# Optimization experiments

Measured on AMD Instinct MI355X. Metric: run time of the kernel, lower is better.

Reference implementation:

```python
import jax, jax.numpy as jnp
import numpy as np

B, S, D, H = 2, 2048, 1024, 16
HD = D // H  # head dim = 64

def setup_inputs() -> dict:
    key = jax.random.key(0)
    k1, k2, k3 = jax.random.split(key, 3)
    return {
        "hidden_state": jax.random.normal(k1, (B, S, D), dtype=jnp.float32),
        "attention_mask": jnp.ones((B, S), dtype=jnp.float32),
        "w_attn": jax.random.normal(k2, (D, 3 * D), dtype=jnp.float32) * 0.02,
        "b_attn": jnp.zeros((3 * D,), dtype=jnp.float32),
        "w_proj": jax.random.normal(k3, (D, D), dtype=jnp.float32) * 0.02,
        "b_proj": jnp.zeros((D,), dtype=jnp.float32),
    }

def reference(hidden_state, attention_mask, w_attn, b_attn, w_proj, b_proj):
    x = hidden_state  # [B,S,D]
    # Conv1D: F.linear(x, weight.T, bias) == x @ weight + bias
    qkv = x @ w_attn + b_attn  # [B,S,3D]
    q, k, v = jnp.split(qkv, 3, axis=-1)
    def heads(t):  # [B,S,D] -> [B,H,S,HD]
        return t.reshape(B, S, H, HD).transpose(0, 2, 1, 3)
    q, k, v = heads(q), heads(k), heads(v)
    # scaled scores
    scores = jnp.einsum("bhqd,bhkd->bhqk", q, k) / jnp.sqrt(jnp.float32(HD))
    # mask: expand (B,S)->(B,S,S) along keys, tril, 1-that, !=0 -> -inf
    m = jnp.broadcast_to(attention_mask[:, None, :], (B, S, S))
    neg = 1.0 - jnp.tril(m)  # nonzero where disallowed
    bias = jnp.where(neg != 0.0, -jnp.inf, 0.0)  # [B,S,S]
    scores = scores + bias[:, None, :, :]
    attn = jax.nn.softmax(scores, axis=-1)  # [B,H,S,S] (dropout p=0)
    ctx = jnp.einsum("bhqk,bhkd->bhqd", attn, v)  # [B,H,S,HD]
    ctx = ctx.transpose(0, 2, 1, 3).reshape(B, S, D)
    out = ctx @ w_proj + b_proj  # resid dropout p=0
    # original returns attention.transpose(0,1): (H,B,S,S)->(B,H,S,S)
    return out, attn
```

## Files before the change

kernel.cpp:

```cpp
#include <hip/hip_runtime.h>

#define S_ 2048
#define D_ 1024
#define H_ 16
#define HD_ 64

typedef __attribute__((ext_vector_type(8))) short short8;
typedef __attribute__((ext_vector_type(4))) float floatx4;

#define MFMA16(a, b, c) __builtin_amdgcn_mfma_f32_16x16x32_bf16(a, b, c, 0, 0, 0)

__device__ inline unsigned short f2bf(float f) {
    union { float f; unsigned int u; } v; v.f = f;
    unsigned int r = v.u + 0x7FFFu + ((v.u >> 16) & 1u);
    return (unsigned short)(r >> 16);
}

__global__ __launch_bounds__(256) void cast_bf16(const float* __restrict__ in,
                                                 unsigned short* __restrict__ out, int n4) {
    int i = blockIdx.x * 256 + threadIdx.x;
    if (i < n4) {
        float4 v = ((const float4*)in)[i];
        ushort4 o;
        o.x = f2bf(v.x); o.y = f2bf(v.y); o.z = f2bf(v.z); o.w = f2bf(v.w);
        ((ushort4*)out)[i] = o;
    }
}

__global__ __launch_bounds__(256) void transpose_cast(const float* __restrict__ W,
                                                      unsigned short* __restrict__ WT,
                                                      int K, int N) {
    __shared__ float tb[64][65];
    const int t = threadIdx.x;
    const int tr = t >> 4, tc = t & 15;
    const int n0 = blockIdx.x * 64, k0 = blockIdx.y * 64;
#pragma unroll
    for (int p = 0; p < 4; ++p) {
        const int r = p * 16 + tr;
        const float4 v = *(const float4*)&W[(size_t)(k0 + r) * N + n0 + tc * 4];
        tb[r][tc * 4 + 0] = v.x; tb[r][tc * 4 + 1] = v.y;
        tb[r][tc * 4 + 2] = v.z; tb[r][tc * 4 + 3] = v.w;
    }
    __syncthreads();
#pragma unroll
    for (int p = 0; p < 4; ++p) {
        const int rn = p * 16 + tr;
        ushort4 o;
        o.x = f2bf(tb[tc * 4 + 0][rn]); o.y = f2bf(tb[tc * 4 + 1][rn]);
        o.z = f2bf(tb[tc * 4 + 2][rn]); o.w = f2bf(tb[tc * 4 + 3][rn]);
        *(ushort4*)&WT[(size_t)(n0 + rn) * K + k0 + tc * 4] = o;
    }
}

__global__ __launch_bounds__(256) void gemm_bt(
    const unsigned short* __restrict__ A, const unsigned short* __restrict__ Bt,
    const float* __restrict__ bias, float* __restrict__ outp,
    unsigned short* __restrict__ qw, unsigned short* __restrict__ kw,
    unsigned short* __restrict__ vtw, int M, int N, int K, int mode)
{
    __shared__ unsigned short As[128 * 32];
    __shared__ unsigned short Bs[128 * 32];

    const int tid = threadIdx.x;
    const int w = tid >> 6, lane = tid & 63;
    const int l15 = lane & 15, qd = lane >> 4;
    const int wr = w >> 1, wc = w & 1;
    const int row0 = blockIdx.y * 128, col0 = blockIdx.x * 128;

    floatx4 acc[4][4];
#pragma unroll
    for (int i = 0; i < 4; ++i)
#pragma unroll
        for (int j = 0; j < 4; ++j) acc[i][j] = (floatx4){0.f, 0.f, 0.f, 0.f};

    for (int k0 = 0; k0 < K; k0 += 32) {
        __syncthreads();
#pragma unroll
        for (int p = 0; p < 2; ++p) {
            const int c = p * 256 + tid;
            const int row = c >> 2, part = c & 3;
            *(uint4*)&As[row * 32 + part * 8] =
                *(const uint4*)&A[(size_t)(row0 + row) * K + k0 + part * 8];
            *(uint4*)&Bs[row * 32 + part * 8] =
                *(const uint4*)&Bt[(size_t)(col0 + row) * K + k0 + part * 8];
        }
        __syncthreads();
        short8 af[4], bfr[4];
#pragma unroll
        for (int mi = 0; mi < 4; ++mi)
            af[mi] = *(const short8*)&As[(wr * 64 + mi * 16 + l15) * 32 + qd * 8];
#pragma unroll
        for (int ni = 0; ni < 4; ++ni)
            bfr[ni] = *(const short8*)&Bs[(wc * 64 + ni * 16 + l15) * 32 + qd * 8];
#pragma unroll
        for (int mi = 0; mi < 4; ++mi)
#pragma unroll
            for (int ni = 0; ni < 4; ++ni)
                acc[mi][ni] = MFMA16(af[mi], bfr[ni], acc[mi][ni]);
    }

#pragma unroll
    for (int mi = 0; mi < 4; ++mi)
#pragma unroll
        for (int ni = 0; ni < 4; ++ni) {
            const int col = col0 + wc * 64 + ni * 16 + l15;
            const float bv = bias[col];
#pragma unroll
            for (int r = 0; r < 4; ++r) {
                const int row = row0 + wr * 64 + mi * 16 + qd * 4 + r;
                const float v = acc[mi][ni][r] + bv;
                if (mode == 0) {
                    outp[(size_t)row * N + col] = v;
                } else {
                    const int region = col >> 10;
                    const int hh = (col >> 6) & 15;
                    const int dd = col & 63;
                    const int bb = row >> 11;
                    const int ss = row & 2047;
                    const unsigned short bvv = f2bf(v);
                    if (region == 0)
                        qw[((size_t)(bb * 16 + hh) * 2048 + ss) * 64 + dd] = bvv;
                    else if (region == 1)
                        kw[((size_t)(bb * 16 + hh) * 2048 + ss) * 64 + dd] = bvv;
                    else
                        vtw[((size_t)(bb * 16 + hh) * 64 + dd) * 2048 + ss] = bvv;
                }
            }
        }
}

__global__ __launch_bounds__(256) void attn_mfma(
    const unsigned short* __restrict__ qg, const unsigned short* __restrict__ kg,
    const unsigned short* __restrict__ vtg, const float* __restrict__ mask,
    float* __restrict__ attnOut, unsigned short* __restrict__ ctxOut)
{
    __shared__ unsigned short Qs[64 * 72];
    __shared__ unsigned short Ks[64 * 72];
    __shared__ unsigned short Vt[64 * 72];
    __shared__ unsigned short Ps[64 * 80];
    __shared__ float maskS[64];

    const int tid = threadIdx.x;
    const int w = tid >> 6, lane = tid & 63;
    const int l15 = lane & 15, qd = lane >> 4;
    const int x = blockIdx.x;
    const int bh = x & 31;
    const int qt = 31 - (x >> 5);
    const int b = bh >> 4, h = bh & 15;
    const size_t base = (size_t)bh * (S_ * HD_);

#pragma unroll
    for (int p = 0; p < 2; ++p) {
        const int c = p * 256 + tid;
        const int row = c >> 3, part = c & 7;
        *(uint4*)&Qs[row * 72 + part * 8] =
            *(const uint4*)&qg[base + (size_t)(qt * 64 + row) * 64 + part * 8];
    }
    __syncthreads();
    const short8 aq0 = *(const short8*)&Qs[(w * 16 + l15) * 72 + 0 + qd * 8];
    const short8 aq1 = *(const short8*)&Qs[(w * 16 + l15) * 72 + 32 + qd * 8];

    const int qrow_base = qt * 64 + w * 16 + qd * 4;
    float m_i[4], l_i[4], rl[4];
#pragma unroll
    for (int r = 0; r < 4; ++r) { m_i[r] = -3e38f; l_i[r] = 0.f; }

    for (int jt = 0; jt <= qt; ++jt) {
        __syncthreads();
#pragma unroll
        for (int p = 0; p < 2; ++p) {
            const int c = p * 256 + tid;
            const int row = c >> 3, part = c & 7;
            *(uint4*)&Ks[row * 72 + part * 8] =
                *(const uint4*)&kg[base + (size_t)(jt * 64 + row) * 64 + part * 8];
        }
        if (tid < 64) maskS[tid] = mask[b * S_ + jt * 64 + tid];
        __syncthreads();

        float sv[4][4];
#pragma unroll
        for (int ni = 0; ni < 4; ++ni) {
            const short8 bk0 = *(const short8*)&Ks[(ni * 16 + l15) * 72 + 0 + qd * 8];
            const short8 bk1 = *(const short8*)&Ks[(ni * 16 + l15) * 72 + 32 + qd * 8];
            floatx4 s = {0.f, 0.f, 0.f, 0.f};
            s = MFMA16(aq0, bk0, s);
            s = MFMA16(aq1, bk1, s);
#pragma unroll
            for (int r = 0; r < 4; ++r) sv[ni][r] = s[r] * 0.125f;
        }
#pragma unroll
        for (int r = 0; r < 4; ++r) {
            const int qrow = qrow_base + r;
            float svr[4], tm = -3e38f;
#pragma unroll
            for (int ni = 0; ni < 4; ++ni) {
                const int col = jt * 64 + ni * 16 + l15;
                const bool ok = (col <= qrow) && (maskS[ni * 16 + l15] == 1.0f);
                svr[ni] = ok ? sv[ni][r] : -3e38f;
                tm = fmaxf(tm, svr[ni]);
            }
            if (tm > -1e37f) {
                const float mn = fmaxf(m_i[r], tm);
                const float sum = __expf(svr[0] - mn) + __expf(svr[1] - mn) +
                                  __expf(svr[2] - mn) + __expf(svr[3] - mn);
                l_i[r] = l_i[r] * __expf(m_i[r] - mn) + sum;
                m_i[r] = mn;
            }
        }
    }

#pragma unroll
    for (int r = 0; r < 4; ++r) {
        float m = m_i[r], l = l_i[r];
#pragma unroll
        for (int off = 1; off < 16; off <<= 1) {
            const float mo = __shfl_xor(m, off);
            const float lo = __shfl_xor(l, off);
            const float mn = fmaxf(m, mo);
            l = l * __expf(m - mn) + lo * __expf(mo - mn);
            m = mn;
        }
        m_i[r] = m;
        rl[r] = 1.0f / l;
    }

    floatx4 ctxa[4];
#pragma unroll
    for (int ni = 0; ni < 4; ++ni) ctxa[ni] = (floatx4){0.f, 0.f, 0.f, 0.f};
    float* attnBH = attnOut + (size_t)bh * S_ * S_;

    for (int jt = 0; jt < 32; ++jt) {
        if (jt <= qt) {
            __syncthreads();
#pragma unroll
            for (int p = 0; p < 2; ++p) {
                const int c = p * 256 + tid;
                const int row = c >> 3, part = c & 7;
                *(uint4*)&Ks[row * 72 + part * 8] =
                    *(const uint4*)&kg[base + (size_t)(jt * 64 + row) * 64 + part * 8];
                *(uint4*)&Vt[row * 72 + part * 8] =
                    *(const uint4*)&vtg[base + (size_t)row * S_ + jt * 64 + part * 8];
            }
            if (tid < 64) maskS[tid] = mask[b * S_ + jt * 64 + tid];
            __syncthreads();

            float sv[4][4];
#pragma unroll
            for (int ni = 0; ni < 4; ++ni) {
                const short8 bk0 = *(const short8*)&Ks[(ni * 16 + l15) * 72 + 0 + qd * 8];
                const short8 bk1 = *(const short8*)&Ks[(ni * 16 + l15) * 72 + 32 + qd * 8];
                floatx4 s = {0.f, 0.f, 0.f, 0.f};
                s = MFMA16(aq0, bk0, s);
                s = MFMA16(aq1, bk1, s);
#pragma unroll
                for (int r = 0; r < 4; ++r) sv[ni][r] = s[r] * 0.125f;
            }
#pragma unroll
            for (int ni = 0; ni < 4; ++ni) {
#pragma unroll
                for (int r = 0; r < 4; ++r) {
                    const int qrow = qrow_base + r;
                    const int col = jt * 64 + ni * 16 + l15;
                    const bool ok = (col <= qrow) && (maskS[ni * 16 + l15] == 1.0f);
                    const float p = ok ? __expf(sv[ni][r] - m_i[r]) * rl[r] : 0.0f;
                    attnBH[(size_t)qrow * S_ + col] = p;
                    Ps[(w * 16 + qd * 4 + r) * 80 + ni * 16 + l15] = f2bf(p);
                }
            }
            __syncthreads();
#pragma unroll
            for (int kk = 0; kk < 2; ++kk) {
                const short8 ap = *(const short8*)&Ps[(w * 16 + l15) * 80 + kk * 32 + qd * 8];
#pragma unroll
                for (int ni = 0; ni < 4; ++ni) {
                    const short8 bv = *(const short8*)&Vt[(ni * 16 + l15) * 72 + kk * 32 + qd * 8];
                    ctxa[ni] = MFMA16(ap, bv, ctxa[ni]);
                }
            }
        } else {
            const float4 z = {0.f, 0.f, 0.f, 0.f};
#pragma unroll
            for (int p = 0; p < 4; ++p) {
                const int c = p * 256 + tid;
                const int row = c >> 4, part = c & 15;
                *(float4*)&attnBH[(size_t)(qt * 64 + row) * S_ + jt * 64 + part * 4] = z;
            }
        }
    }

#pragma unroll
    for (int ni = 0; ni < 4; ++ni)
#pragma unroll
        for (int r = 0; r < 4; ++r) {
            const int qrow = qrow_base + r;
            ctxOut[((size_t)(b * S_ + qrow)) * D_ + h * 64 + ni * 16 + l15] =
                f2bf(ctxa[ni][r]);
        }
}

extern "C" void kernel_launch(void* const* d_in, const int* in_sizes, int n_in,
                              void* d_out, int out_size, void* d_ws, size_t ws_size,
                              hipStream_t stream) {
    const float* hidden = (const float*)d_in[0];
    const float* mask   = (const float*)d_in[1];
    const float* w_attn = (const float*)d_in[2];
    const float* b_attn = (const float*)d_in[3];
    const float* w_proj = (const float*)d_in[4];
    const float* b_proj = (const float*)d_in[5];

    float* out = (float*)d_out;
    float* attnOut = out + (size_t)2 * S_ * D_;

    unsigned short* ws = (unsigned short*)d_ws;
    const size_t E = (size_t)2 * S_ * D_;
    unsigned short* Xb   = ws;
    unsigned short* WaT  = Xb + E;
    unsigned short* WpT  = WaT + (size_t)3 * D_ * D_;
    unsigned short* qw   = WpT + (size_t)D_ * D_;
    unsigned short* kw   = qw + E;
    unsigned short* vtw  = kw + E;
    unsigned short* ctxb = vtw + E;

    dim3 blk(256);
    cast_bf16<<<dim3((int)(E / 4 / 256)), blk, 0, stream>>>(hidden, Xb, (int)(E / 4));
    transpose_cast<<<dim3(3 * D_ / 64, D_ / 64), blk, 0, stream>>>(w_attn, WaT, D_, 3 * D_);
    transpose_cast<<<dim3(D_ / 64, D_ / 64), blk, 0, stream>>>(w_proj, WpT, D_, D_);

    gemm_bt<<<dim3(3 * D_ / 128, 2 * S_ / 128), blk, 0, stream>>>(
        Xb, WaT, b_attn, nullptr, qw, kw, vtw, 2 * S_, 3 * D_, D_, 1);

    attn_mfma<<<dim3(2 * H_ * (S_ / 64)), blk, 0, stream>>>(
        qw, kw, vtw, mask, attnOut, ctxb);

    gemm_bt<<<dim3(D_ / 128, 2 * S_ / 128), blk, 0, stream>>>(
        ctxb, WpT, b_proj, out, nullptr, nullptr, nullptr, 2 * S_, D_, D_, 0);
}
```

Before: 748.6 us.

## Double-buffer GEMM and attention tiles via direct global-to-LDS loads with swizzle

Replaces register-staged shared-memory loads in the GEMM and attention kernels with global_load_lds direct copies into double-buffered, XOR-swizzled LDS tiles. The next K/V tile is prefetched while the current one is computed. Softmax switches to exp2 with a log2e-folded scale, and the causal compare is skipped off the diagonal tile. The large attention-probability and output writes become nontemporal stores, and MFMA sections get raised wave priority. These aim to hide global-load latency and cut LDS bank conflicts and write-cache pollution. The cost is extra LDS use and reliance on correct async-load synchronization.

After: 740.3 us. Within noise of the previous version (-1.1%).

```diff
diff --git a/kernel.cpp b/kernel.cpp
--- a/kernel.cpp
+++ b/kernel.cpp
@@ -9,11 +9,18 @@
 typedef __attribute__((ext_vector_type(4))) float floatx4;
 
 #define MFMA16(a, b, c) __builtin_amdgcn_mfma_f32_16x16x32_bf16(a, b, c, 0, 0, 0)
-
-__device__ inline unsigned short f2bf(float f) {
+#define EXP2 __builtin_amdgcn_exp2f
+
+__device__ __forceinline__ unsigned short f2bf(float f) {
     union { float f; unsigned int u; } v; v.f = f;
     unsigned int r = v.u + 0x7FFFu + ((v.u >> 16) & 1u);
     return (unsigned short)(r >> 16);
+}
+
+__device__ __forceinline__ void gll16(const unsigned short* g, unsigned short* l) {
+    __builtin_amdgcn_global_load_lds(
+        (const __attribute__((address_space(1))) void*)g,
+        (__attribute__((address_space(3))) void*)l, 16, 0, 0);
 }
 
 __global__ __launch_bounds__(256) void cast_bf16(const float* __restrict__ in,
@@ -58,8 +65,8 @@
     unsigned short* __restrict__ qw, unsigned short* __restrict__ kw,
     unsigned short* __restrict__ vtw, int M, int N, int K, int mode)
 {
-    __shared__ unsigned short As[128 * 32];
-    __shared__ unsigned short Bs[128 * 32];
+    __shared__ unsigned short As[2][128 * 32];
+    __shared__ unsigned short Bs[2][128 * 32];
 
     const int tid = threadIdx.x;
     const int w = tid >> 6, lane = tid & 63;
@@ -73,25 +80,38 @@
 #pragma unroll
         for (int j = 0; j < 4; ++j) acc[i][j] = (floatx4){0.f, 0.f, 0.f, 0.f};
 
-    for (int k0 = 0; k0 < K; k0 += 32) {
+    const int sr = tid >> 2;
+    const int gs = (tid & 3) ^ ((tid >> 3) & 3);
+    const unsigned short* Ab0 = A + (size_t)(row0 + sr) * K + gs * 8;
+    const unsigned short* Ab1 = A + (size_t)(row0 + 64 + sr) * K + gs * 8;
+    const unsigned short* Bb0 = Bt + (size_t)(col0 + sr) * K + gs * 8;
+    const unsigned short* Bb1 = Bt + (size_t)(col0 + 64 + sr) * K + gs * 8;
+
+    auto stage = [&](int bi, int k0) {
+        gll16(Ab0 + k0, &As[bi][tid * 8]);
+        gll16(Ab1 + k0, &As[bi][(256 + tid) * 8]);
+        gll16(Bb0 + k0, &Bs[bi][tid * 8]);
+        gll16(Bb1 + k0, &Bs[bi][(256 + tid) * 8]);
+    };
+
+    stage(0, 0);
+    const int nk = K >> 5;
+    for (int it = 0; it < nk; ++it) {
         __syncthreads();
-#pragma unroll
-        for (int p = 0; p < 2; ++p) {
-            const int c = p * 256 + tid;
-            const int row = c >> 2, part = c & 3;
-            *(uint4*)&As[row * 32 + part * 8] =
-                *(const uint4*)&A[(size_t)(row0 + row) * K + k0 + part * 8];
-            *(uint4*)&Bs[row * 32 + part * 8] =
-                *(const uint4*)&Bt[(size_t)(col0 + row) * K + k0 + part * 8];
-        }
-        __syncthreads();
+        if (it + 1 < nk) stage((it + 1) & 1, (it + 1) << 5);
+        const unsigned short* Asb = As[it & 1];
+        const unsigned short* Bsb = Bs[it & 1];
         short8 af[4], bfr[4];
 #pragma unroll
-        for (int mi = 0; mi < 4; ++mi)
-            af[mi] = *(const short8*)&As[(wr * 64 + mi * 16 + l15) * 32 + qd * 8];
-#pragma unroll
-        for (int ni = 0; ni < 4; ++ni)
-            bfr[ni] = *(const short8*)&Bs[(wc * 64 + ni * 16 + l15) * 32 + qd * 8];
+        for (int mi = 0; mi < 4; ++mi) {
+            const int ra = wr * 64 + mi * 16 + l15;
+            af[mi] = *(const short8*)&Asb[ra * 32 + ((qd ^ ((ra >> 1) & 3)) << 3)];
+        }
+#pragma unroll
+        for (int ni = 0; ni < 4; ++ni) {
+            const int rb = wc * 64 + ni * 16 + l15;
+            bfr[ni] = *(const short8*)&Bsb[rb * 32 + ((qd ^ ((rb >> 1) & 3)) << 3)];
+        }
 #pragma unroll
         for (int mi = 0; mi < 4; ++mi)
 #pragma unroll
@@ -110,7 +130,7 @@
                 const int row = row0 + wr * 64 + mi * 16 + qd * 4 + r;
                 const float v = acc[mi][ni][r] + bv;
                 if (mode == 0) {
-                    outp[(size_t)row * N + col] = v;
+                    __builtin_nontemporal_store(v, &outp[(size_t)row * N + col]);
                 } else {
                     const int region = col >> 10;
                     const int hh = (col >> 6) & 15;
@@ -134,11 +154,11 @@
     const unsigned short* __restrict__ vtg, const float* __restrict__ mask,
     float* __restrict__ attnOut, unsigned short* __restrict__ ctxOut)
 {
-    __shared__ unsigned short Qs[64 * 72];
-    __shared__ unsigned short Ks[64 * 72];
-    __shared__ unsigned short Vt[64 * 72];
+    __shared__ unsigned short Qb[64 * 64];
+    __shared__ unsigned short Kb[2][64 * 64];
+    __shared__ unsigned short Vb[2][64 * 64];
     __shared__ unsigned short Ps[64 * 80];
-    __shared__ float maskS[64];
+    __shared__ float maskS[2][64];
 
     const int tid = threadIdx.x;
     const int w = tid >> 6, lane = tid & 63;
@@ -148,17 +168,35 @@
     const int qt = 31 - (x >> 5);
     const int b = bh >> 4, h = bh & 15;
     const size_t base = (size_t)bh * (S_ * HD_);
-
-#pragma unroll
-    for (int p = 0; p < 2; ++p) {
-        const int c = p * 256 + tid;
-        const int row = c >> 3, part = c & 7;
-        *(uint4*)&Qs[row * 72 + part * 8] =
-            *(const uint4*)&qg[base + (size_t)(qt * 64 + row) * 64 + part * 8];
-    }
+    const float SC = 0.18033688f;
+
+    const int sr = tid >> 3;
+    const int sp = tid & 7;
+    const int gsw = sp ^ (sr & 7);
+
+    auto stageK = [&](int bi, int jt) {
+        const unsigned short* gk = kg + base + (size_t)jt * 4096;
+        gll16(gk + sr * 64 + gsw * 8, &Kb[bi][tid * 8]);
+        gll16(gk + (sr + 32) * 64 + gsw * 8, &Kb[bi][(256 + tid) * 8]);
+    };
+    auto stageV = [&](int bi, int jt) {
+        const unsigned short* gv = vtg + base + jt * 64;
+        gll16(gv + (size_t)sr * S_ + gsw * 8, &Vb[bi][tid * 8]);
+        gll16(gv + (size_t)(sr + 32) * S_ + gsw * 8, &Vb[bi][(256 + tid) * 8]);
+    };
+
+    {
+        const unsigned short* gq = qg + base + (size_t)qt * 4096;
+        gll16(gq + sr * 64 + gsw * 8, &Qb[tid * 8]);
+        gll16(gq + (sr + 32) * 64 + gsw * 8, &Qb[(256 + tid) * 8]);
+    }
+    stageK(0, 0);
+    if (tid < 64) maskS[0][tid] = mask[b * S_ + tid];
     __syncthreads();
-    const short8 aq0 = *(const short8*)&Qs[(w * 16 + l15) * 72 + 0 + qd * 8];
-    const short8 aq1 = *(const short8*)&Qs[(w * 16 + l15) * 72 + 32 + qd * 8];
+
+    const int qr = w * 16 + l15;
+    const short8 aq0 = *(const short8*)&Qb[qr * 64 + ((qd ^ (qr & 7)) << 3)];
+    const short8 aq1 = *(const short8*)&Qb[qr * 64 + (((4 + qd) ^ (qr & 7)) << 3)];
 
     const int qrow_base = qt * 64 + w * 16 + qd * 4;
     float m_i[4], l_i[4], rl[4];
@@ -166,47 +204,47 @@
     for (int r = 0; r < 4; ++r) { m_i[r] = -3e38f; l_i[r] = 0.f; }
 
     for (int jt = 0; jt <= qt; ++jt) {
-        __syncthreads();
-#pragma unroll
-        for (int p = 0; p < 2; ++p) {
-            const int c = p * 256 + tid;
-            const int row = c >> 3, part = c & 7;
-            *(uint4*)&Ks[row * 72 + part * 8] =
-                *(const uint4*)&kg[base + (size_t)(jt * 64 + row) * 64 + part * 8];
-        }
-        if (tid < 64) maskS[tid] = mask[b * S_ + jt * 64 + tid];
-        __syncthreads();
-
+        const int cb = jt & 1;
+        if (jt < qt) {
+            stageK(cb ^ 1, jt + 1);
+            if (tid < 64) maskS[cb ^ 1][tid] = mask[b * S_ + (jt + 1) * 64 + tid];
+        }
         float sv[4][4];
+        bool mok[4];
+        __builtin_amdgcn_s_setprio(1);
 #pragma unroll
         for (int ni = 0; ni < 4; ++ni) {
-            const short8 bk0 = *(const short8*)&Ks[(ni * 16 + l15) * 72 + 0 + qd * 8];
-            const short8 bk1 = *(const short8*)&Ks[(ni * 16 + l15) * 72 + 32 + qd * 8];
+            const int kr = ni * 16 + l15;
+            const short8 bk0 = *(const short8*)&Kb[cb][kr * 64 + ((qd ^ (kr & 7)) << 3)];
+            const short8 bk1 = *(const short8*)&Kb[cb][kr * 64 + (((4 + qd) ^ (kr & 7)) << 3)];
             floatx4 s = {0.f, 0.f, 0.f, 0.f};
             s = MFMA16(aq0, bk0, s);
             s = MFMA16(aq1, bk1, s);
 #pragma unroll
-            for (int r = 0; r < 4; ++r) sv[ni][r] = s[r] * 0.125f;
-        }
+            for (int r = 0; r < 4; ++r) sv[ni][r] = s[r] * SC;
+            mok[ni] = (maskS[cb][kr] == 1.0f);
+        }
+        __builtin_amdgcn_s_setprio(0);
+        const bool diag = (jt == qt);
 #pragma unroll
         for (int r = 0; r < 4; ++r) {
             const int qrow = qrow_base + r;
             float svr[4], tm = -3e38f;
 #pragma unroll
             for (int ni = 0; ni < 4; ++ni) {
-                const int col = jt * 64 + ni * 16 + l15;
-                const bool ok = (col <= qrow) && (maskS[ni * 16 + l15] == 1.0f);
+                const bool ok = mok[ni] && (!diag || (jt * 64 + ni * 16 + l15 <= qrow));
                 svr[ni] = ok ? sv[ni][r] : -3e38f;
                 tm = fmaxf(tm, svr[ni]);
             }
             if (tm > -1e37f) {
                 const float mn = fmaxf(m_i[r], tm);
-                const float sum = __expf(svr[0] - mn) + __expf(svr[1] - mn) +
-                                  __expf(svr[2] - mn) + __expf(svr[3] - mn);
-                l_i[r] = l_i[r] * __expf(m_i[r] - mn) + sum;
+                const float sum = EXP2(svr[0] - mn) + EXP2(svr[1] - mn) +
+                                  EXP2(svr[2] - mn) + EXP2(svr[3] - mn);
+                l_i[r] = l_i[r] * EXP2(m_i[r] - mn) + sum;
                 m_i[r] = mn;
             }
         }
+        __syncthreads();
     }
 
 #pragma unroll
@@ -217,13 +255,17 @@
             const float mo = __shfl_xor(m, off);
             const float lo = __shfl_xor(l, off);
             const float mn = fmaxf(m, mo);
-            l = l * __expf(m - mn) + lo * __expf(mo - mn);
+            l = l * EXP2(m - mn) + lo * EXP2(mo - mn);
             m = mn;
         }
         m_i[r] = m;
         rl[r] = 1.0f / l;
     }
 
+    stageK(0, 0);
+    stageV(0, 0);
+    if (tid < 64) maskS[0][tid] = mask[b * S_ + tid];
+
     floatx4 ctxa[4];
 #pragma unroll
     for (int ni = 0; ni < 4; ++ni) ctxa[ni] = (floatx4){0.f, 0.f, 0.f, 0.f};
@@ -231,59 +273,69 @@
 
     for (int jt = 0; jt < 32; ++jt) {
         if (jt <= qt) {
+            const int cb = jt & 1;
             __syncthreads();
-#pragma unroll
-            for (int p = 0; p < 2; ++p) {
-                const int c = p * 256 + tid;
-                const int row = c >> 3, part = c & 7;
-                *(uint4*)&Ks[row * 72 + part * 8] =
-                    *(const uint4*)&kg[base + (size_t)(jt * 64 + row) * 64 + part * 8];
-                *(uint4*)&Vt[row * 72 + part * 8] =
-                    *(const uint4*)&vtg[base + (size_t)row * S_ + jt * 64 + part * 8];
-            }
-            if (tid < 64) maskS[tid] = mask[b * S_ + jt * 64 + tid];
-            __syncthreads();
-
-            float sv[4][4];
+            if (jt < qt) {
+                stageK(cb ^ 1, jt + 1);
+                stageV(cb ^ 1, jt + 1);
+                if (tid < 64) maskS[cb ^ 1][tid] = mask[b * S_ + (jt + 1) * 64 + tid];
+            }
+            float pm[4][4];
+            bool mok[4];
+            __builtin_amdgcn_s_setprio(1);
 #pragma unroll
             for (int ni = 0; ni < 4; ++ni) {
-                const short8 bk0 = *(const short8*)&Ks[(ni * 16 + l15) * 72 + 0 + qd * 8];
-                const short8 bk1 = *(const short8*)&Ks[(ni * 16 + l15) * 72 + 32 + qd * 8];
+                const int kr = ni * 16 + l15;
+                const short8 bk0 = *(const short8*)&Kb[cb][kr * 64 + ((qd ^ (kr & 7)) << 3)];
+                const short8 bk1 = *(const short8*)&Kb[cb][kr * 64 + (((4 + qd) ^ (kr & 7)) << 3)];
                 floatx4 s = {0.f, 0.f, 0.f, 0.f};
                 s = MFMA16(aq0, bk0, s);
                 s = MFMA16(aq1, bk1, s);
 #pragma unroll
-                for (int r = 0; r < 4; ++r) sv[ni][r] = s[r] * 0.125f;
-            }
-#pragma unroll
-            for (int ni = 0; ni < 4; ++ni) {
+                for (int r = 0; r < 4; ++r) pm[ni][r] = s[r] * SC;
+                mok[ni] = (maskS[cb][kr] == 1.0f);
+            }
+            __builtin_amdgcn_s_setprio(0);
+            const bool diag = (jt == qt);
+#pragma unroll
+            for (int ni = 0; ni < 4; ++ni)
 #pragma unroll
                 for (int r = 0; r < 4; ++r) {
                     const int qrow = qrow_base + r;
-                    const int col = jt * 64 + ni * 16 + l15;
-                    const bool ok = (col <= qrow) && (maskS[ni * 16 + l15] == 1.0f);
-                    const float p = ok ? __expf(sv[ni][r] - m_i[r]) * rl[r] : 0.0f;
-                    attnBH[(size_t)qrow * S_ + col] = p;
+                    const bool ok = mok[ni] && (!diag || (jt * 64 + ni * 16 + l15 <= qrow));
+                    const float p = ok ? EXP2(pm[ni][r] - m_i[r]) * rl[r] : 0.0f;
+                    pm[ni][r] = p;
                     Ps[(w * 16 + qd * 4 + r) * 80 + ni * 16 + l15] = f2bf(p);
                 }
-            }
             __syncthreads();
+#pragma unroll
+            for (int ni = 0; ni < 4; ++ni)
+#pragma unroll
+                for (int r = 0; r < 4; ++r)
+                    __builtin_nontemporal_store(
+                        pm[ni][r],
+                        &attnBH[(size_t)(qrow_base + r) * S_ + jt * 64 + ni * 16 + l15]);
+            __builtin_amdgcn_s_setprio(1);
 #pragma unroll
             for (int kk = 0; kk < 2; ++kk) {
                 const short8 ap = *(const short8*)&Ps[(w * 16 + l15) * 80 + kk * 32 + qd * 8];
 #pragma unroll
                 for (int ni = 0; ni < 4; ++ni) {
-                    const short8 bv = *(const short8*)&Vt[(ni * 16 + l15) * 72 + kk * 32 + qd * 8];
+                    const int vr = ni * 16 + l15;
+                    const short8 bv = *(const short8*)
+                        &Vb[cb][vr * 64 + (((kk * 4 + qd) ^ (vr & 7)) << 3)];
                     ctxa[ni] = MFMA16(ap, bv, ctxa[ni]);
                 }
             }
+            __builtin_amdgcn_s_setprio(0);
         } else {
-            const float4 z = {0.f, 0.f, 0.f, 0.f};
+            const floatx4 z = {0.f, 0.f, 0.f, 0.f};
 #pragma unroll
             for (int p = 0; p < 4; ++p) {
                 const int c = p * 256 + tid;
                 const int row = c >> 4, part = c & 15;
-                *(float4*)&attnBH[(size_t)(qt * 64 + row) * S_ + jt * 64 + part * 4] = z;
+                __builtin_nontemporal_store(
+                    z, (floatx4*)&attnBH[(size_t)(qt * 64 + row) * S_ + jt * 64 + part * 4]);
             }
         }
     }
```
